# Kernel tuning notes

Measured on AMD Instinct MI355X. Metric: run time of the kernel, lower is better.

## Reference

```python
import jax, jax.numpy as jnp
import numpy as np

N, E, D, NUM_REL, NUM_LAYERS = 20000, 100000, 768, 7, 5  # 6 edge types + self-loop relation


def setup_inputs() -> dict:
    key = jax.random.key(0)
    ks = jax.random.split(key, 8)
    x = jax.random.normal(ks[0], (N, D), dtype=jnp.float32)
    edge_index = jax.random.randint(ks[1], (2, E), 0, N, dtype=jnp.int64)
    # original edge_type values are in [-1, 5]; module adds 1 -> [0, 6]
    edge_type = jax.random.randint(ks[2], (E,), -1, 6, dtype=jnp.int64)
    scale = 1.0 / np.sqrt(D)
    weights = jax.random.normal(ks[3], (NUM_LAYERS, NUM_REL, D, D), dtype=jnp.float32) * scale
    roots = jax.random.normal(ks[4], (NUM_LAYERS, D, D), dtype=jnp.float32) * scale
    biases = jax.random.normal(ks[5], (NUM_LAYERS, D), dtype=jnp.float32) * 0.01
    return {"x": x, "edge_index": edge_index, "edge_type": edge_type,
            "weights": weights, "roots": roots, "biases": biases}


def _rgcn_conv(h, src, dst, safe_et, W, root, b):
    # PyG RGCNConv (aggr='mean', root_weight=True, bias=True):
    #   out = x @ root + b + sum_r mean_{edges of rel r into v}(x[src]) @ W_r
    n = h.shape[0]
    hs = h[src]  # [E, D] gather once, reused across relations
    out = h @ root + b
    for r in range(NUM_REL):
        m = (safe_et == r).astype(h.dtype)  # [E]
        msg_sum = jax.ops.segment_sum(hs * m[:, None], dst, num_segments=n)  # [N, D]
        cnt = jax.ops.segment_sum(m, dst, num_segments=n)  # [N]
        mean = msg_sum / jnp.maximum(cnt, 1.0)[:, None]  # zero where no rel-r edges
        out = out + mean @ W[r]
    return out


def reference(x, edge_index, edge_type, weights, roots, biases):
    src, dst = edge_index[0], edge_index[1]
    safe_et = edge_type + 1  # [-1..5] -> [0..6]
    h = x
    for l in range(NUM_LAYERS):
        h = _rgcn_conv(h, src, dst, safe_et, weights[l], roots[l], biases[l])
        h = jax.nn.relu(h)  # dropout=0 -> identity
    return h
```

## Files before the change

### kernel.cpp

```cpp
#include <hip/hip_runtime.h>

typedef unsigned short u16;
typedef unsigned int   u32;
typedef __attribute__((ext_vector_type(8))) short short8;
typedef __attribute__((ext_vector_type(4))) float f32x4;

#define DD      768
#define KK      6144
#define NREL    7
#define NLAYERS 5

__device__ __forceinline__ float b2f(u16 v) {
  return __uint_as_float(((u32)v) << 16);
}
__device__ __forceinline__ u16 f2bf(float f) {
  u32 x = __float_as_uint(f);
  x += 0x7fffu + ((x >> 16) & 1u);
  return (u16)(x >> 16);
}
__device__ __forceinline__ void gload16(const void* g, void* l) {
  __builtin_amdgcn_global_load_lds(
      (const __attribute__((address_space(1))) void*)g,
      (__attribute__((address_space(3))) void*)l, 16, 0, 0);
}


__global__ void cast_x_kernel(const float* __restrict__ x, u16* __restrict__ H, size_t n) {
  for (size_t i = ((size_t)blockIdx.x * 256 + threadIdx.x) * 4; i < n; i += (size_t)gridDim.x * 256 * 4) {
    float4 v = *(const float4*)&x[i];
    u32 lo = (u32)f2bf(v.x) | ((u32)f2bf(v.y) << 16);
    u32 hi = (u32)f2bf(v.z) | ((u32)f2bf(v.w) << 16);
    uint2 o; o.x = lo; o.y = hi;
    *(uint2*)&H[i] = o;
  }
}

__global__ void count_kernel(const int* __restrict__ eidx, const int* __restrict__ etype,
                             int* cnt_dst, int* cnt_rel, int E, int Nn) {
  int e = blockIdx.x * 256 + threadIdx.x;
  if (e >= E) return;
  int dst = eidx[E + e];
  int rel = etype[e] + 1;
  atomicAdd(&cnt_dst[dst], 1);
  atomicAdd(&cnt_rel[(size_t)rel * Nn + dst], 1);
}

__global__ __launch_bounds__(1024) void scan_kernel(const int* __restrict__ cnt, int* __restrict__ offs, int n) {
  __shared__ int part[1024];
  int t = threadIdx.x;
  int per = (n + 1023) / 1024;
  int base = t * per;
  int s = 0;
  for (int i = 0; i < per; ++i) { int idx = base + i; if (idx < n) s += cnt[idx]; }
  part[t] = s;
  __syncthreads();
  for (int o = 1; o < 1024; o <<= 1) {
    int v = (t >= o) ? part[t - o] : 0;
    __syncthreads();
    part[t] += v;
    __syncthreads();
  }
  int excl = (t == 0) ? 0 : part[t - 1];
  s = excl;
  for (int i = 0; i < per; ++i) { int idx = base + i; if (idx < n) { offs[idx] = s; s += cnt[idx]; } }
  if (t == 1023) offs[n] = part[1023];
}

__global__ void fillperm_kernel(const int* __restrict__ eidx, const int* __restrict__ offs,
                                int* fill, int* perm, int E) {
  int e = blockIdx.x * 256 + threadIdx.x;
  if (e >= E) return;
  int dst = eidx[E + e];
  int pos = offs[dst] + atomicAdd(&fill[dst], 1);
  perm[pos] = e;
}

__global__ void wcat_kernel(const float* __restrict__ W, const float* __restrict__ R, u16* __restrict__ Bt) {
  __shared__ float t[32 * 33];
  int b = blockIdx.x;
  int s = b / 576, rem = b % 576;
  int kt = rem / 24, nt = rem % 24;
  const float* src = (s == 0) ? R : (W + (size_t)(s - 1) * DD * DD);
  int tj = threadIdx.x & 31, ti = threadIdx.x >> 5;
#pragma unroll
  for (int i = 0; i < 4; ++i) {
    int kk = kt * 32 + ti + i * 8;
    t[(ti + i * 8) * 33 + tj] = src[(size_t)kk * DD + nt * 32 + tj];
  }
  __syncthreads();
#pragma unroll
  for (int i = 0; i < 4; ++i) {
    int nn_ = nt * 32 + ti + i * 8;
    Bt[(size_t)nn_ * KK + (size_t)s * DD + kt * 32 + tj] = f2bf(t[tj * 33 + ti + i * 8]);
  }
}

__global__ __launch_bounds__(192) void aggregate_kernel(
    const u16* __restrict__ H, const int* __restrict__ esrc, const int* __restrict__ etype,
    const int* __restrict__ offs, const int* __restrict__ perm, const int* __restrict__ cnt_rel,
    u16* __restrict__ Acat, int node0, int Nn) {
  int v = node0 + blockIdx.x;
  int t = threadIdx.x;
  int j0 = t * 4;
  size_t rowbase = (size_t)blockIdx.x * KK;
  *(uint2*)&Acat[rowbase + j0] = *(const uint2*)&H[(size_t)v * DD + j0];
  float a0[4] = {0,0,0,0}, a1[4] = {0,0,0,0}, a2[4] = {0,0,0,0}, a3[4] = {0,0,0,0};
  float a4[4] = {0,0,0,0}, a5[4] = {0,0,0,0}, a6[4] = {0,0,0,0};
  int beg = offs[v], end = offs[v + 1];
  for (int e = beg; e < end; ++e) {
    int eid = perm[e];
    int src = esrc[eid];
    int rel = etype[eid] + 1;
    uint2 w = *(const uint2*)&H[(size_t)src * DD + j0];
    float f0 = b2f((u16)(w.x & 0xffff));
    float f1 = b2f((u16)(w.x >> 16));
    float f2 = b2f((u16)(w.y & 0xffff));
    float f3 = b2f((u16)(w.y >> 16));
    switch (rel) {
      case 0: a0[0]+=f0; a0[1]+=f1; a0[2]+=f2; a0[3]+=f3; break;
      case 1: a1[0]+=f0; a1[1]+=f1; a1[2]+=f2; a1[3]+=f3; break;
      case 2: a2[0]+=f0; a2[1]+=f1; a2[2]+=f2; a2[3]+=f3; break;
      case 3: a3[0]+=f0; a3[1]+=f1; a3[2]+=f2; a3[3]+=f3; break;
      case 4: a4[0]+=f0; a4[1]+=f1; a4[2]+=f2; a4[3]+=f3; break;
      case 5: a5[0]+=f0; a5[1]+=f1; a5[2]+=f2; a5[3]+=f3; break;
      default: a6[0]+=f0; a6[1]+=f1; a6[2]+=f2; a6[3]+=f3; break;
    }
  }
  const float* regs[NREL] = {a0, a1, a2, a3, a4, a5, a6};
#pragma unroll
  for (int r = 0; r < NREL; ++r) {
    int c = cnt_rel[(size_t)r * Nn + v];
    float inv = (c > 0) ? 1.f / (float)c : 0.f;
    const float* a = regs[r];
    u32 lo = (u32)f2bf(a[0] * inv) | ((u32)f2bf(a[1] * inv) << 16);
    u32 hi = (u32)f2bf(a[2] * inv) | ((u32)f2bf(a[3] * inv) << 16);
    uint2 o; o.x = lo; o.y = hi;
    *(uint2*)&Acat[rowbase + (size_t)(r + 1) * DD + j0] = o;
  }
}


#define MFMA_(a_, b_, c_) __builtin_amdgcn_mfma_f32_16x16x32_bf16(a_, b_, c_, 0, 0, 0)
#define BAR   __builtin_amdgcn_s_barrier()
#define SCB   __builtin_amdgcn_sched_barrier(0)
#define VM8   asm volatile("s_waitcnt vmcnt(8)" ::: "memory")
#define VM0   asm volatile("s_waitcnt vmcnt(0)" ::: "memory")

__global__ __launch_bounds__(256, 1) void gemm4w_kernel(
    const u16* __restrict__ A, const u16* __restrict__ Bt, const float* __restrict__ bias,
    u16* __restrict__ Hout, float* __restrict__ Cout, int Mvalid, int Mtiles) {
  __shared__ char smA[4][16384];
  __shared__ char smB[4][16384];

  int tid = threadIdx.x;
  int lane = tid & 63;
  int wv = tid >> 6;
  int wm = wv >> 1, wn = wv & 1;

  int nwg = Mtiles * 3;
  int orig = (int)blockIdx.x;
  int q8 = nwg >> 3, r8 = nwg & 7;
  int xcd = orig & 7, rank = orig >> 3;
  int wg = (xcd < r8 ? xcd * (q8 + 1) : r8 * (q8 + 1) + (xcd - r8) * q8) + rank;
  int bm = wg / 3, bn = wg % 3;

  int srow = tid >> 2;
  int sch = (tid & 3) ^ ((tid >> 3) & 3);
  const char* gA[4];
  const char* gB[4];
#pragma unroll
  for (int j = 0; j < 4; ++j) {
    int ra = bm * 256 + j * 64 + srow;
    if (ra > Mvalid - 1) ra = Mvalid - 1;
    gA[j] = (const char*)A  + (size_t)ra * (KK * 2) + sch * 16;
    gB[j] = (const char*)Bt + (size_t)(bn * 256 + j * 64 + srow) * (KK * 2) + sch * 16;
  }
  int rsel = lane & 15, kq = lane >> 4;
  int loff = rsel * 64 + ((kq ^ ((rsel >> 1) & 3)) * 16);

  f32x4 acc[8][8];
#pragma unroll
  for (int m = 0; m < 8; ++m)
#pragma unroll
    for (int n = 0; n < 8; ++n) acc[m][n] = (f32x4){0.f, 0.f, 0.f, 0.f};

#define STAGE(st, s_)                                                     \
  do {                                                                    \
    size_t ko_ = (size_t)(st) * 64;                                       \
    gload16(gA[0] + ko_, &smA[s_][tid * 16]);                             \
    gload16(gA[1] + ko_, &smA[s_][4096 + tid * 16]);                      \
    gload16(gA[2] + ko_, &smA[s_][8192 + tid * 16]);                      \
    gload16(gA[3] + ko_, &smA[s_][12288 + tid * 16]);                     \
    gload16(gB[0] + ko_, &smB[s_][tid * 16]);                             \
    gload16(gB[1] + ko_, &smB[s_][4096 + tid * 16]);                      \
    gload16(gB[2] + ko_, &smB[s_][8192 + tid * 16]);                      \
    gload16(gB[3] + ko_, &smB[s_][12288 + tid * 16]);                     \
  } while (0)

#define READF(s_, AR, BR)                                                 \
  do {                                                                    \
    _Pragma("unroll")                                                     \
    for (int m_ = 0; m_ < 8; ++m_)                                        \
      AR[m_] = *(const short8*)(&smA[s_][(wm * 128 + m_ * 16) * 64 + loff]); \
    _Pragma("unroll")                                                     \
    for (int n_ = 0; n_ < 8; ++n_)                                        \
      BR[n_] = *(const short8*)(&smB[s_][(wn * 128 + n_ * 16) * 64 + loff]); \
  } while (0)

#define MFMA64(AR, BR)                                                    \
  do {                                                                    \
    _Pragma("unroll")                                                     \
    for (int m_ = 0; m_ < 8; ++m_)                                        \
      _Pragma("unroll")                                                   \
      for (int n_ = 0; n_ < 8; ++n_)                                      \
        acc[m_][n_] = MFMA_(AR[m_], BR[n_], acc[m_][n_]);                 \
  } while (0)

#define HALF(sSt, sSl, rSl, RA, RB, MA, MB)                               \
  do {                                                                    \
    STAGE(sSt, sSl);                                                      \
    VM8; BAR; SCB;                                                        \
    READF(rSl, RA, RB);                                                   \
    MFMA64(MA, MB);                                                       \
  } while (0)

  short8 aE[8], bE[8], aO[8], bO[8];

  STAGE(0, 0);
  STAGE(1, 1);
  VM8; BAR; SCB;
  READF(0, aE, bE);

  for (int t = 0; t < 188; t += 4) {
    HALF(t + 2, 2, 1, aO, bO, aE, bE);
    HALF(t + 3, 3, 2, aE, bE, aO, bO);
    HALF(t + 4, 0, 3, aO, bO, aE, bE);
    HALF(t + 5, 1, 0, aE, bE, aO, bO);
  }
  HALF(190, 2, 1, aO, bO, aE, bE);
  HALF(191, 3, 2, aE, bE, aO, bO);
  VM0; BAR; SCB;
  READF(3, aO, bO);
  MFMA64(aE, bE);
  MFMA64(aO, bO);

#undef HALF
#undef MFMA64
#undef READF
#undef STAGE

  int rif = (lane >> 4) * 4;
  int cidx = lane & 15;
#pragma unroll
  for (int m = 0; m < 8; ++m) {
    int rl = bm * 256 + wm * 128 + m * 16 + rif;
#pragma unroll
    for (int n = 0; n < 8; ++n) {
      int c = bn * 256 + wn * 128 + n * 16 + cidx;
      float bv = bias[c];
#pragma unroll
      for (int j = 0; j < 4; ++j) {
        int r = rl + j;
        if (r < Mvalid) {
          float v = acc[m][n][j] + bv;
          v = v > 0.f ? v : 0.f;
          if (Hout) Hout[(size_t)r * DD + c] = f2bf(v);
          if (Cout) Cout[(size_t)r * DD + c] = v;
        }
      }
    }
  }
}


static inline size_t alignup(size_t x, size_t a) { return (x + a - 1) & ~(a - 1); }

extern "C" void kernel_launch(void* const* d_in, const int* in_sizes, int n_in,
                              void* d_out, int out_size, void* d_ws, size_t ws_size,
                              hipStream_t stream) {
  const float* x       = (const float*)d_in[0];
  const int*   eidx    = (const int*)d_in[1];
  const int*   etype   = (const int*)d_in[2];
  const float* weights = (const float*)d_in[3];
  const float* roots   = (const float*)d_in[4];
  const float* biases  = (const float*)d_in[5];
  float* out = (float*)d_out;

  const int Nn = in_sizes[0] / DD;
  const int E  = in_sizes[2];

  char* p = (char*)d_ws;
  size_t off = 0;
  auto carve = [&](size_t bytes) -> char* {
    char* r = p + off;
    off = alignup(off + bytes, 256);
    return r;
  };
  u16* H0      = (u16*)carve((size_t)Nn * DD * 2);
  u16* Bt      = (u16*)carve((size_t)DD * KK * 2);
  int* cnt_rel = (int*)carve((size_t)NREL * Nn * 4);
  int* cnt_dst = (int*)carve((size_t)Nn * 4);
  int* offs    = (int*)carve((size_t)(Nn + 1) * 4);
  int* fill    = (int*)carve((size_t)Nn * 4);
  int* perm    = (int*)carve((size_t)E * 4);

  size_t rem = (ws_size > off) ? (ws_size - off) : 0;
  int McCap = (int)(rem / ((size_t)KK * 2));
  int Mpad = ((Nn + 255) / 256) * 256;
  int Mc = (McCap < Mpad) ? (McCap & ~255) : Mpad;
  if (Mc < 256) return;
  u16* Acat = (u16*)(p + off);
  int nchunks = (Nn + Mc - 1) / Mc;
  u16* H1 = (u16*)d_out;

  (void)hipMemsetAsync(cnt_rel, 0, (size_t)NREL * Nn * 4, stream);
  (void)hipMemsetAsync(cnt_dst, 0, (size_t)Nn * 4, stream);
  (void)hipMemsetAsync(fill, 0, (size_t)Nn * 4, stream);

  int eg = (E + 255) / 256;
  count_kernel<<<eg, 256, 0, stream>>>(eidx, etype, cnt_dst, cnt_rel, E, Nn);
  scan_kernel<<<1, 1024, 0, stream>>>(cnt_dst, offs, Nn);
  fillperm_kernel<<<eg, 256, 0, stream>>>(eidx, offs, fill, perm, E);
  cast_x_kernel<<<2048, 256, 0, stream>>>(x, H0, (size_t)Nn * DD);

  const u16* Hin = H0;
  u16* Hnext = H1;
  for (int l = 0; l < NLAYERS; ++l) {
    wcat_kernel<<<8 * 576, 256, 0, stream>>>(weights + (size_t)l * NREL * DD * DD,
                                             roots + (size_t)l * DD * DD, Bt);
    for (int c = 0; c < nchunks; ++c) {
      int node0 = c * Mc;
      int nn = (Nn - node0 < Mc) ? (Nn - node0) : Mc;
      aggregate_kernel<<<nn, 192, 0, stream>>>(Hin, eidx, etype, offs, perm, cnt_rel,
                                               Acat, node0, Nn);
      int mt = (nn + 255) / 256;
      u16* ho = (l < NLAYERS - 1) ? (Hnext + (size_t)node0 * DD) : nullptr;
      float* co = (l == NLAYERS - 1) ? (out + (size_t)node0 * DD) : nullptr;
      gemm4w_kernel<<<mt * 3, 256, 0, stream>>>(Acat, Bt, biases + (size_t)l * DD, ho, co, nn, mt);
    }
    const u16* t_ = Hin;
    Hin = Hnext;
    Hnext = (u16*)t_;
  }
}
```

Before: 1.653 ms.

## Pre-swizzle weights into MFMA fragment layout and load B directly to registers

The weight concat kernel now writes B in a fragment-ordered layout, so each lane can load its bf16 MFMA operand for a 16-column group straight from global memory with one 16-byte load. The GEMM drops the B shared-memory buffers, moves to 512 threads (8 waves, 2x4 wave grid with 8x4 accumulator tiles per wave), and double-buffers B in registers while A still streams through a four-slot LDS ring. It also raises MFMA priority with setprio and reorders block-to-tile mapping so blocks sharing an N-column stripe are grouped. This aims to cut LDS traffic and register pressure, but it relies on B being served well from L2 with no LDS reuse across the M waves.

Result: no change. 1.660 ms (+0.4%).

```diff
diff --git a/kernel.cpp b/kernel.cpp
--- a/kernel.cpp
+++ b/kernel.cpp
@@ -75,7 +75,7 @@
   perm[pos] = e;
 }
 
-__global__ void wcat_kernel(const float* __restrict__ W, const float* __restrict__ R, u16* __restrict__ Bt) {
+__global__ void wcat_kernel(const float* __restrict__ W, const float* __restrict__ R, u16* __restrict__ Bn) {
   __shared__ float t[32 * 33];
   int b = blockIdx.x;
   int s = b / 576, rem = b % 576;
@@ -88,10 +88,13 @@
     t[(ti + i * 8) * 33 + tj] = src[(size_t)kk * DD + nt * 32 + tj];
   }
   __syncthreads();
+  int kkidx = s * 24 + kt;
+  int kq = tj >> 3, e = tj & 7;
 #pragma unroll
   for (int i = 0; i < 4; ++i) {
-    int nn_ = nt * 32 + ti + i * 8;
-    Bt[(size_t)nn_ * KK + (size_t)s * DD + kt * 32 + tj] = f2bf(t[tj * 33 + ti + i * 8]);
+    int n = nt * 32 + ti + i * 8;
+    size_t idx = ((size_t)(n >> 4) * 192 + kkidx) * 512 + (size_t)(kq * 16 + (n & 15)) * 8 + e;
+    Bn[idx] = f2bf(t[tj * 33 + ti + i * 8]);
   }
 }
 
@@ -142,111 +145,104 @@
 
 #define MFMA_(a_, b_, c_) __builtin_amdgcn_mfma_f32_16x16x32_bf16(a_, b_, c_, 0, 0, 0)
 #define BAR   __builtin_amdgcn_s_barrier()
-#define SCB   __builtin_amdgcn_sched_barrier(0)
-#define VM8   asm volatile("s_waitcnt vmcnt(8)" ::: "memory")
+#define VM6   asm volatile("s_waitcnt vmcnt(6)" ::: "memory")
+#define VM4   asm volatile("s_waitcnt vmcnt(4)" ::: "memory")
 #define VM0   asm volatile("s_waitcnt vmcnt(0)" ::: "memory")
 
-__global__ __launch_bounds__(256, 1) void gemm4w_kernel(
-    const u16* __restrict__ A, const u16* __restrict__ Bt, const float* __restrict__ bias,
+__global__ __launch_bounds__(512, 1) void gemmhy_kernel(
+    const u16* __restrict__ A, const u16* __restrict__ Bn, const float* __restrict__ bias,
     u16* __restrict__ Hout, float* __restrict__ Cout, int Mvalid, int Mtiles) {
   __shared__ char smA[4][16384];
-  __shared__ char smB[4][16384];
 
   int tid = threadIdx.x;
   int lane = tid & 63;
   int wv = tid >> 6;
-  int wm = wv >> 1, wn = wv & 1;
+  int wm = wv >> 2, wn = wv & 3;
 
   int nwg = Mtiles * 3;
   int orig = (int)blockIdx.x;
   int q8 = nwg >> 3, r8 = nwg & 7;
   int xcd = orig & 7, rank = orig >> 3;
   int wg = (xcd < r8 ? xcd * (q8 + 1) : r8 * (q8 + 1) + (xcd - r8) * q8) + rank;
-  int bm = wg / 3, bn = wg % 3;
-
-  int srow = tid >> 2;
+  int bm = wg % Mtiles, bn = wg / Mtiles;
+
   int sch = (tid & 3) ^ ((tid >> 3) & 3);
-  const char* gA[4];
-  const char* gB[4];
-#pragma unroll
-  for (int j = 0; j < 4; ++j) {
-    int ra = bm * 256 + j * 64 + srow;
+  const char* gA[2];
+#pragma unroll
+  for (int j = 0; j < 2; ++j) {
+    int ra = bm * 256 + j * 128 + (tid >> 2);
     if (ra > Mvalid - 1) ra = Mvalid - 1;
-    gA[j] = (const char*)A  + (size_t)ra * (KK * 2) + sch * 16;
-    gB[j] = (const char*)Bt + (size_t)(bn * 256 + j * 64 + srow) * (KK * 2) + sch * 16;
+    gA[j] = (const char*)A + (size_t)ra * (KK * 2) + sch * 16;
   }
   int rsel = lane & 15, kq = lane >> 4;
-  int loff = rsel * 64 + ((kq ^ ((rsel >> 1) & 3)) * 16);
-
-  f32x4 acc[8][8];
+  int loff = rsel * 64 + ((kq ^ ((rsel >> 1) & 3)) * 16) + wm * 8192;
+
+  const char* pb[4];
+#pragma unroll
+  for (int n = 0; n < 4; ++n)
+    pb[n] = (const char*)Bn + ((size_t)(bn * 16 + wn * 4 + n) * 192) * 1024 + lane * 16;
+
+  f32x4 acc[8][4];
 #pragma unroll
   for (int m = 0; m < 8; ++m)
 #pragma unroll
-    for (int n = 0; n < 8; ++n) acc[m][n] = (f32x4){0.f, 0.f, 0.f, 0.f};
-
-#define STAGE(st, s_)                                                     \
+    for (int n = 0; n < 4; ++n) acc[m][n] = (f32x4){0.f, 0.f, 0.f, 0.f};
+
+#define STAGE(T2, SL)                                                     \
   do {                                                                    \
-    size_t ko_ = (size_t)(st) * 64;                                       \
-    gload16(gA[0] + ko_, &smA[s_][tid * 16]);                             \
-    gload16(gA[1] + ko_, &smA[s_][4096 + tid * 16]);                      \
-    gload16(gA[2] + ko_, &smA[s_][8192 + tid * 16]);                      \
-    gload16(gA[3] + ko_, &smA[s_][12288 + tid * 16]);                     \
-    gload16(gB[0] + ko_, &smB[s_][tid * 16]);                             \
-    gload16(gB[1] + ko_, &smB[s_][4096 + tid * 16]);                      \
-    gload16(gB[2] + ko_, &smB[s_][8192 + tid * 16]);                      \
-    gload16(gB[3] + ko_, &smB[s_][12288 + tid * 16]);                     \
+    size_t ko_ = (size_t)(T2) * 64;                                       \
+    gload16(gA[0] + ko_, &smA[SL][tid * 16]);                             \
+    gload16(gA[1] + ko_, &smA[SL][8192 + tid * 16]);                      \
   } while (0)
 
-#define READF(s_, AR, BR)                                                 \
+#define LOADB(T2, BR)                                                     \
   do {                                                                    \
+    size_t bo_ = (size_t)(T2) * 1024;                                     \
+    BR[0] = *(const short8*)(pb[0] + bo_);                                \
+    BR[1] = *(const short8*)(pb[1] + bo_);                                \
+    BR[2] = *(const short8*)(pb[2] + bo_);                                \
+    BR[3] = *(const short8*)(pb[3] + bo_);                                \
+  } while (0)
+
+#define KSTEP(T, SL, CURB, NXTB, DO_STG, DO_BLD, VMW)                     \
+  do {                                                                    \
+    BAR;                                                                  \
+    short8 aF[8];                                                         \
     _Pragma("unroll")                                                     \
     for (int m_ = 0; m_ < 8; ++m_)                                        \
-      AR[m_] = *(const short8*)(&smA[s_][(wm * 128 + m_ * 16) * 64 + loff]); \
-    _Pragma("unroll")                                                     \
-    for (int n_ = 0; n_ < 8; ++n_)                                        \
-      BR[n_] = *(const short8*)(&smB[s_][(wn * 128 + n_ * 16) * 64 + loff]); \
-  } while (0)
-
-#define MFMA64(AR, BR)                                                    \
-  do {                                                                    \
+      aF[m_] = *(const short8*)(&smA[SL][m_ * 1024 + loff]);              \
+    if (DO_STG) STAGE((T) + 2, ((SL) + 2) & 3);                           \
+    if (DO_BLD) LOADB((T) + 1, NXTB);                                     \
+    VMW;                                                                  \
+    __builtin_amdgcn_s_setprio(1);                                        \
     _Pragma("unroll")                                                     \
     for (int m_ = 0; m_ < 8; ++m_)                                        \
       _Pragma("unroll")                                                   \
-      for (int n_ = 0; n_ < 8; ++n_)                                      \
-        acc[m_][n_] = MFMA_(AR[m_], BR[n_], acc[m_][n_]);                 \
+      for (int n_ = 0; n_ < 4; ++n_)                                      \
+        acc[m_][n_] = MFMA_(aF[m_], CURB[n_], acc[m_][n_]);               \
+    __builtin_amdgcn_s_setprio(0);                                        \
   } while (0)
 
-#define HALF(sSt, sSl, rSl, RA, RB, MA, MB)                               \
-  do {                                                                    \
-    STAGE(sSt, sSl);                                                      \
-    VM8; BAR; SCB;                                                        \
-    READF(rSl, RA, RB);                                                   \
-    MFMA64(MA, MB);                                                       \
-  } while (0)
-
-  short8 aE[8], bE[8], aO[8], bO[8];
+  short8 bE[4], bO[4];
 
   STAGE(0, 0);
   STAGE(1, 1);
-  VM8; BAR; SCB;
-  READF(0, aE, bE);
+  LOADB(0, bE);
+  VM6;
 
   for (int t = 0; t < 188; t += 4) {
-    HALF(t + 2, 2, 1, aO, bO, aE, bE);
-    HALF(t + 3, 3, 2, aE, bE, aO, bO);
-    HALF(t + 4, 0, 3, aO, bO, aE, bE);
-    HALF(t + 5, 1, 0, aE, bE, aO, bO);
-  }
-  HALF(190, 2, 1, aO, bO, aE, bE);
-  HALF(191, 3, 2, aE, bE, aO, bO);
-  VM0; BAR; SCB;
-  READF(3, aO, bO);
-  MFMA64(aE, bE);
-  MFMA64(aO, bO);
-
-#undef HALF
-#undef MFMA64
-#undef READF
+    KSTEP(t + 0, 0, bE, bO, 1, 1, VM6);
+    KSTEP(t + 1, 1, bO, bE, 1, 1, VM6);
+    KSTEP(t + 2, 2, bE, bO, 1, 1, VM6);
+    KSTEP(t + 3, 3, bO, bE, 1, 1, VM6);
+  }
+  KSTEP(188, 0, bE, bO, 1, 1, VM6);
+  KSTEP(189, 1, bO, bE, 1, 1, VM6);
+  KSTEP(190, 2, bE, bO, 0, 1, VM4);
+  KSTEP(191, 3, bO, bE, 0, 0, VM0);
+
+#undef KSTEP
+#undef LOADB
 #undef STAGE
 
   int rif = (lane >> 4) * 4;
@@ -255,8 +251,8 @@
   for (int m = 0; m < 8; ++m) {
     int rl = bm * 256 + wm * 128 + m * 16 + rif;
 #pragma unroll
-    for (int n = 0; n < 8; ++n) {
-      int c = bn * 256 + wn * 128 + n * 16 + cidx;
+    for (int n = 0; n < 4; ++n) {
+      int c = bn * 256 + wn * 64 + n * 16 + cidx;
       float bv = bias[c];
 #pragma unroll
       for (int j = 0; j < 4; ++j) {
@@ -297,7 +293,7 @@
     return r;
   };
   u16* H0      = (u16*)carve((size_t)Nn * DD * 2);
-  u16* Bt      = (u16*)carve((size_t)DD * KK * 2);
+  u16* Bn      = (u16*)carve((size_t)DD * KK * 2);
   int* cnt_rel = (int*)carve((size_t)NREL * Nn * 4);
   int* cnt_dst = (int*)carve((size_t)Nn * 4);
   int* offs    = (int*)carve((size_t)(Nn + 1) * 4);
@@ -327,7 +323,7 @@
   u16* Hnext = H1;
   for (int l = 0; l < NLAYERS; ++l) {
     wcat_kernel<<<8 * 576, 256, 0, stream>>>(weights + (size_t)l * NREL * DD * DD,
-                                             roots + (size_t)l * DD * DD, Bt);
+                                             roots + (size_t)l * DD * DD, Bn);
     for (int c = 0; c < nchunks; ++c) {
       int node0 = c * Mc;
       int nn = (Nn - node0 < Mc) ? (Nn - node0) : Mc;
@@ -336,7 +332,7 @@
       int mt = (nn + 255) / 256;
       u16* ho = (l < NLAYERS - 1) ? (Hnext + (size_t)node0 * DD) : nullptr;
       float* co = (l == NLAYERS - 1) ? (out + (size_t)node0 * DD) : nullptr;
-      gemm4w_kernel<<<mt * 3, 256, 0, stream>>>(Acat, Bt, biases + (size_t)l * DD, ho, co, nn, mt);
+      gemmhy_kernel<<<mt * 3, 512, 0, stream>>>(Acat, Bn, biases + (size_t)l * DD, ho, co, nn, mt);
     }
     const u16* t_ = Hin;
     Hin = Hnext;
```
